# Kernel optimization log

Hardware: AMD Instinct MI355X
Metric: run time of the kernel (lower is better)

The kernel has to match this reference:

```python
import jax, jax.numpy as jnp
import numpy as np

B, N, K, F, L, H, ZMAX = 16, 1024, 16, 128, 4, 128, 100


def setup_inputs() -> dict:
    key = jax.random.key(0)
    ks = jax.random.split(key, 12)
    cell = jnp.eye(3, dtype=jnp.float32)[None] * 8.0 + 0.05 * jax.random.normal(ks[0], (B, 3, 3), dtype=jnp.float32)
    x = jax.random.uniform(ks[1], (B, N, 3), dtype=jnp.float32)
    z = jax.random.randint(ks[2], (B, N), 0, ZMAX)
    struct_size = jnp.full((B,), N, dtype=jnp.int32)
    emb = 0.02 * jax.random.normal(ks[3], (ZMAX, F), dtype=jnp.float32)
    din = 2 * F + 1
    W1 = jax.random.normal(ks[4], (L, din, F), dtype=jnp.float32) / np.sqrt(din)
    b1 = jnp.zeros((L, F), dtype=jnp.float32)
    W2 = jax.random.normal(ks[5], (L, F, F), dtype=jnp.float32) / np.sqrt(F)
    b2 = jnp.zeros((L, F), dtype=jnp.float32)
    A1 = jax.random.normal(ks[6], (din, H), dtype=jnp.float32) / np.sqrt(din)
    a1 = jnp.zeros((H,), dtype=jnp.float32)
    A2 = jax.random.normal(ks[7], (H, 1), dtype=jnp.float32) / np.sqrt(H)
    a2 = jnp.zeros((1,), dtype=jnp.float32)
    return {"cell": cell, "x": x, "z": z, "struct_size": struct_size, "emb": emb,
            "W1": W1, "b1": b1, "W2": W2, "b2": b2, "A1": A1, "a1": a1, "A2": A2, "a2": a2}


def _periodic_knn(cell, frac, k):
    # frac: [B,N,3] fractional coords, cell: [B,3,3] lattice rows.
    b, n, _ = frac.shape
    g = jnp.arange(-1, 2, dtype=frac.dtype)
    shifts = jnp.stack(jnp.meshgrid(g, g, g, indexing="ij"), -1).reshape(-1, 3)  # [27,3]
    rel = frac[:, None, :, :] - frac[:, :, None, :]  # rel[b,i,j] = frac_j - frac_i, [B,N,N,3]

    def body(carry, si):
        bd2, bsi = carry
        s, i = si
        cart = jnp.einsum("bijd,bde->bije", rel + s, cell)
        d2 = jnp.sum(cart * cart, axis=-1)
        upd = d2 < bd2
        return (jnp.where(upd, d2, bd2), jnp.where(upd, i, bsi)), None

    init = (jnp.full((b, n, n), 1e30, dtype=frac.dtype), jnp.zeros((b, n, n), dtype=jnp.int32))
    (d2min, simin), _ = jax.lax.scan(body, init, (shifts, jnp.arange(27, dtype=jnp.int32)))
    eye = jnp.eye(n, dtype=bool)
    d2min = jnp.where(eye[None], 1e30, d2min)  # exclude self (zero-shift) edges
    _, idx = jax.lax.top_k(-d2min, k)  # [B,N,k] neighbor indices
    sid = jnp.take_along_axis(simin, idx, axis=2)  # best image shift per edge
    svec = shifts[sid]  # [B,N,k,3]
    frac_j = jax.vmap(lambda f, i: f[i])(frac, idx)  # [B,N,k,3]
    vec = jnp.einsum("bnkd,bde->bnke", frac_j - frac[:, :, None, :] + svec, cell)
    d = jnp.sqrt(jnp.maximum(jnp.sum(vec * vec, axis=-1), 1e-12))  # [B,N,k]
    return idx, vec, d


def _edge_feat(h, idx, d):
    hj = jax.vmap(lambda hb, ib: hb[ib])(h, idx)  # [B,N,k,F]
    hi = jnp.broadcast_to(h[:, :, None, :], hj.shape)
    return jnp.concatenate([hi, hj, d[..., None]], axis=-1)  # [B,N,k,2F+1]


def reference(cell, x, z, struct_size, emb, W1, b1, W2, b2, A1, a1, A2, a2):
    frac = jnp.mod(x, 1.0)
    idx, vec, d = _periodic_knn(cell, frac, K)
    h = emb[z]  # [B,N,F]
    for l in range(W1.shape[0]):
        feat = _edge_feat(h, idx, d)
        m = jax.nn.silu(feat @ W1[l] + b1[l]) @ W2[l] + b2[l]  # [B,N,k,F]
        h = h + jnp.mean(m, axis=2)
    feat = _edge_feat(h, idx, d)
    w = jax.nn.silu(feat @ A1 + a1) @ A2 + a2  # [B,N,k,1]
    delta_cart = jnp.sum(w * vec, axis=2)  # [B,N,3]
    delta_frac = jnp.einsum("bnd,bde->bne", delta_cart, jnp.linalg.inv(cell))
    return x + delta_frac
```

## Files before the change

kernel.cpp:

```cpp
#include <hip/hip_runtime.h>

#define B_ 16
#define N_ 1024
#define K_ 16
#define F_ 128
#define L_ 4
#define DIN_ 257

typedef __bf16 bf16x8 __attribute__((ext_vector_type(8)));
typedef float f32x4 __attribute__((ext_vector_type(4)));

__device__ __forceinline__ float silu_f(float x) {
    return x / (1.0f + __expf(-x));
}

__device__ __forceinline__ unsigned short f2bf_bits(float f) {
    unsigned u = __builtin_bit_cast(unsigned, f);
    return (unsigned short)((u + 0x7FFFu + ((u >> 16) & 1u)) >> 16);
}

__global__ __launch_bounds__(256) void k_prep(const int* __restrict__ z,
                                              const float* __restrict__ emb,
                                              const float* __restrict__ W1,
                                              const float* __restrict__ W2,
                                              const float* __restrict__ A1,
                                              float* __restrict__ h,
                                              unsigned short* __restrict__ hbf,
                                              unsigned short* __restrict__ Wt1,
                                              unsigned short* __restrict__ Wt2,
                                              unsigned short* __restrict__ At1) {
    int gid = blockIdx.x * 256 + threadIdx.x;
    int id = gid;
    if (id < L_ * 256 * 128) {
        int k = id & 127, n = (id >> 7) & 255, l = id >> 15;
        float v = (n < 128) ? W1[(size_t)l * DIN_ * F_ + (size_t)k * F_ + n]
                            : W1[(size_t)l * DIN_ * F_ + (size_t)(128 + k) * F_ + (n - 128)];
        Wt1[id] = f2bf_bits(v);
    } else {
        int id2 = id - L_ * 256 * 128;
        if (id2 < L_ * 128 * 128) {
            int k = id2 & 127, n = (id2 >> 7) & 127, l = id2 >> 14;
            Wt2[id2] = f2bf_bits(W2[(size_t)l * F_ * F_ + (size_t)k * F_ + n]);
        } else {
            int id3 = id2 - L_ * 128 * 128;
            if (id3 < 256 * 128) {
                int k = id3 & 127, n = id3 >> 7;
                float v = (n < 128) ? A1[(size_t)k * 128 + n]
                                    : A1[(size_t)(128 + k) * 128 + (n - 128)];
                At1[id3] = f2bf_bits(v);
            }
        }
    }
    {
        int t = gid;
        int node = t >> 5;
        int f4 = (t & 31) << 2;
        int zi = z[node];
        float4 v = *reinterpret_cast<const float4*>(&emb[zi * F_ + f4]);
        *reinterpret_cast<float4*>(&h[node * F_ + f4]) = v;
        ushort4 pk;
        pk.x = f2bf_bits(v.x); pk.y = f2bf_bits(v.y);
        pk.z = f2bf_bits(v.z); pk.w = f2bf_bits(v.w);
        *reinterpret_cast<ushort4*>(&hbf[node * F_ + f4]) = pk;
    }
}

__global__ __launch_bounds__(256) void k_knng(const float* __restrict__ x,
                                              const float* __restrict__ cell,
                                              int* __restrict__ idx_o,
                                              float* __restrict__ vec_o,
                                              float* __restrict__ d_o,
                                              const unsigned short* __restrict__ hbf,
                                              const unsigned short* __restrict__ Wt1,
                                              float* __restrict__ uv0) {
    __shared__ float fr[N_ * 3];
    int tid = threadIdx.x;
    int gb = blockIdx.x;
    int batch = gb >> 6;
    int ib = gb & 63;
    const float* xb = x + batch * N_ * 3;
    for (int u = tid; u < N_ * 3; u += 256) {
        float xv = xb[u];
        fr[u] = xv - floorf(xv);
    }
    __syncthreads();
    int wave = tid >> 6;
    int lane = tid & 63;
    int fr16 = lane & 15, ko = lane >> 4;

    const float* cb = cell + batch * 9;
    float c00 = cb[0], c01 = cb[1], c02 = cb[2];
    float c10 = cb[3], c11 = cb[4], c12 = cb[5];
    float c20 = cb[6], c21 = cb[7], c22 = cb[8];

    for (int r4 = 0; r4 < 4; ++r4) {
        int i = ib * 16 + wave * 4 + r4;
        float fi0 = fr[i * 3 + 0], fi1 = fr[i * 3 + 1], fi2 = fr[i * 3 + 2];

        unsigned long long k[16];
#pragma unroll
        for (int t = 0; t < 16; ++t) {
            int j = t * 64 + lane;
            float r0 = fr[j * 3 + 0] - fi0;
            float r1 = fr[j * 3 + 1] - fi1;
            float r2 = fr[j * 3 + 2] - fi2;
            float s0f = (r0 > 0.f) ? -1.f : 0.f;
            float s1f = (r1 > 0.f) ? -1.f : 0.f;
            float s2f = (r2 > 0.f) ? -1.f : 0.f;
            int sid_base = ((r0 > 0.f) ? 0 : 9) + ((r1 > 0.f) ? 0 : 3) + ((r2 > 0.f) ? 0 : 1);
            float rx0 = r0 + s0f, rx1 = r0 + (s0f + 1.0f);
            float ry0 = r1 + s1f, ry1 = r1 + (s1f + 1.0f);
            float rz0 = r2 + s2f, rz1 = r2 + (s2f + 1.0f);
            float best = 3e38f;
            int bsid = 0;
#pragma unroll
            for (int cbo = 0; cbo < 8; ++cbo) {
                float rs0 = (cbo & 4) ? rx1 : rx0;
                float rs1 = (cbo & 2) ? ry1 : ry0;
                float rs2 = (cbo & 1) ? rz1 : rz0;
                float cx = fmaf(rs2, c20, fmaf(rs1, c10, rs0 * c00));
                float cy = fmaf(rs2, c21, fmaf(rs1, c11, rs0 * c01));
                float cz = fmaf(rs2, c22, fmaf(rs1, c12, rs0 * c02));
                float d2 = fmaf(cz, cz, fmaf(cy, cy, cx * cx));
                int sid = sid_base + ((cbo >> 2) & 1) * 9 + ((cbo >> 1) & 1) * 3 + (cbo & 1);
                if (d2 < best) { best = d2; bsid = sid; }
            }
            if (j == i) best = 3e38f;
            unsigned db = __builtin_bit_cast(unsigned, best);
            k[t] = ((unsigned long long)db << 32) | (unsigned)((j << 5) | bsid);
        }

#define CE_(a, b)                                              \
    {                                                          \
        unsigned long long x_ = k[a], y_ = k[b];               \
        bool s_ = y_ < x_;                                     \
        k[a] = s_ ? y_ : x_;                                   \
        k[b] = s_ ? x_ : y_;                                   \
    }
        CE_(0,1) CE_(2,3) CE_(4,5) CE_(6,7) CE_(8,9) CE_(10,11) CE_(12,13) CE_(14,15)
        CE_(0,2) CE_(1,3) CE_(4,6) CE_(5,7) CE_(8,10) CE_(9,11) CE_(12,14) CE_(13,15)
        CE_(1,2) CE_(5,6) CE_(9,10) CE_(13,14)
        CE_(0,4) CE_(1,5) CE_(2,6) CE_(3,7) CE_(8,12) CE_(9,13) CE_(10,14) CE_(11,15)
        CE_(2,4) CE_(3,5) CE_(10,12) CE_(11,13)
        CE_(1,2) CE_(3,4) CE_(5,6) CE_(9,10) CE_(11,12) CE_(13,14)
        CE_(0,8) CE_(1,9) CE_(2,10) CE_(3,11) CE_(4,12) CE_(5,13) CE_(6,14) CE_(7,15)
        CE_(4,8) CE_(5,9) CE_(6,10) CE_(7,11)
        CE_(2,4) CE_(3,5) CE_(6,8) CE_(7,9) CE_(10,12) CE_(11,13)
        CE_(1,2) CE_(3,4) CE_(5,6) CE_(7,8) CE_(9,10) CE_(11,12) CE_(13,14)
#undef CE_

        unsigned long long sel = 0;
        for (int r = 0; r < 16; ++r) {
            unsigned long long m = k[0];
#pragma unroll
            for (int off = 32; off >= 1; off >>= 1) {
                unsigned long long o = __shfl_xor(m, off);
                if (o < m) m = o;
            }
            if (k[0] == m) {
#pragma unroll
                for (int t = 0; t < 15; ++t) k[t] = k[t + 1];
                k[15] = ~0ull;
            }
            if (lane == r) sel = m;
        }

        if (lane < 16) {
            unsigned pk = (unsigned)sel;
            int j = pk >> 5, sid = pk & 31;
            int s0 = sid / 9 - 1, s1 = (sid / 3) % 3 - 1, s2 = sid % 3 - 1;
            float rs0 = (fr[j * 3 + 0] - fi0) + (float)s0;
            float rs1 = (fr[j * 3 + 1] - fi1) + (float)s1;
            float rs2 = (fr[j * 3 + 2] - fi2) + (float)s2;
            float vx = fmaf(rs2, c20, fmaf(rs1, c10, rs0 * c00));
            float vy = fmaf(rs2, c21, fmaf(rs1, c11, rs0 * c01));
            float vz = fmaf(rs2, c22, fmaf(rs1, c12, rs0 * c02));
            float d2 = fmaf(vz, vz, fmaf(vy, vy, vx * vx));
            float dd = sqrtf(fmaxf(d2, 1e-12f));
            int node = batch * N_ + i;
            int eo = node * K_ + lane;
            idx_o[eo] = j;
            d_o[eo] = dd;
            vec_o[eo * 3 + 0] = vx;
            vec_o[eo * 3 + 1] = vy;
            vec_o[eo * 3 + 2] = vz;
        }
    }

    {
        int t = gb * 4 + wave;
        int mt = t >> 3, nt = t & 7;
        const unsigned short* Ap = hbf + (size_t)(mt * 32 + fr16) * 128 + ko * 8;
        const unsigned short* Bp = Wt1 + (size_t)(nt * 32 + fr16) * 128 + ko * 8;
        bf16x8 a0[4], a1v_[4], b0[4], b1v_[4];
#pragma unroll
        for (int ks = 0; ks < 4; ++ks) {
            a0[ks] = *reinterpret_cast<const bf16x8*>(Ap + ks * 32);
            a1v_[ks] = *reinterpret_cast<const bf16x8*>(Ap + 16 * 128 + ks * 32);
            b0[ks] = *reinterpret_cast<const bf16x8*>(Bp + ks * 32);
            b1v_[ks] = *reinterpret_cast<const bf16x8*>(Bp + 16 * 128 + ks * 32);
        }
        f32x4 acc00 = {0.f, 0.f, 0.f, 0.f}, acc01 = acc00, acc10 = acc00, acc11 = acc00;
#pragma unroll
        for (int ks = 0; ks < 4; ++ks) {
            acc00 = __builtin_amdgcn_mfma_f32_16x16x32_bf16(a0[ks], b0[ks], acc00, 0, 0, 0);
            acc01 = __builtin_amdgcn_mfma_f32_16x16x32_bf16(a0[ks], b1v_[ks], acc01, 0, 0, 0);
            acc10 = __builtin_amdgcn_mfma_f32_16x16x32_bf16(a1v_[ks], b0[ks], acc10, 0, 0, 0);
            acc11 = __builtin_amdgcn_mfma_f32_16x16x32_bf16(a1v_[ks], b1v_[ks], acc11, 0, 0, 0);
        }
        int mrow = mt * 32 + ko * 4;
        int cbase = nt * 32 + fr16;
#define EPI_(FM, FN, ACC)                                                    \
    {                                                                        \
        int cc = cbase + FN * 16;                                            \
        _Pragma("unroll") for (int r = 0; r < 4; ++r) {                      \
            int row = mrow + FM * 16 + r;                                    \
            uv0[(size_t)row * 256 + cc] = ACC[r];                            \
        }                                                                    \
    }
        EPI_(0, 0, acc00) EPI_(0, 1, acc01) EPI_(1, 0, acc10) EPI_(1, 1, acc11)
#undef EPI_
    }
}

__global__ __launch_bounds__(256) void k_layer16(const float* __restrict__ UVin,
                                                 const int* __restrict__ idx,
                                                 const float* __restrict__ nd,
                                                 const float* __restrict__ w1d,
                                                 const float* __restrict__ b1l,
                                                 const unsigned short* __restrict__ W2t,
                                                 const float* __restrict__ b2l,
                                                 float* __restrict__ h,
                                                 const unsigned short* __restrict__ W1n,
                                                 float* __restrict__ UVout) {
    __shared__ unsigned short svl[16][136];
    __shared__ unsigned short hbl[16][136];
    __shared__ int ilds[256];
    __shared__ float dlds[256];
    int tid = threadIdx.x;
    int gb = blockIdx.x;
    int batch = (gb & 7) + 8 * (gb >> 9);
    int ib = (gb >> 3) & 63;
    int node0 = batch * N_ + ib * 16;
    int bbase = batch * N_;
    int wave = tid >> 6, lane = tid & 63;
    int fr16 = lane & 15, ko = lane >> 4;

    ilds[tid] = idx[node0 * K_ + tid];
    dlds[tid] = nd[node0 * K_ + tid];
    __syncthreads();

    {
        int gn = tid >> 4, fc = tid & 15, f0 = fc << 3;
        int node = node0 + gn;
        float u[8], wd[8], bb[8], acc[8];
#pragma unroll
        for (int q = 0; q < 8; q += 4) {
            float4 t = *reinterpret_cast<const float4*>(&UVin[(size_t)node * 256 + f0 + q]);
            u[q] = t.x; u[q + 1] = t.y; u[q + 2] = t.z; u[q + 3] = t.w;
            float4 t2 = *reinterpret_cast<const float4*>(&w1d[f0 + q]);
            wd[q] = t2.x; wd[q + 1] = t2.y; wd[q + 2] = t2.z; wd[q + 3] = t2.w;
            float4 t3 = *reinterpret_cast<const float4*>(&b1l[f0 + q]);
            bb[q] = t3.x; bb[q + 1] = t3.y; bb[q + 2] = t3.z; bb[q + 3] = t3.w;
        }
#pragma unroll
        for (int q = 0; q < 8; ++q) acc[q] = 0.f;
        for (int e = 0; e < K_; ++e) {
            int j = ilds[gn * K_ + e];
            float dd = dlds[gn * K_ + e];
            const float* vp = &UVin[(size_t)(bbase + j) * 256 + 128 + f0];
#pragma unroll
            for (int q = 0; q < 8; q += 4) {
                float4 t = *reinterpret_cast<const float4*>(&vp[q]);
                float v4[4] = {t.x, t.y, t.z, t.w};
#pragma unroll
                for (int w = 0; w < 4; ++w) {
                    float pre = u[q + w] + v4[w] + fmaf(dd, wd[q + w], bb[q + w]);
                    acc[q + w] += silu_f(pre);
                }
            }
        }
        const float inv_k = 1.0f / (float)K_;
        unsigned ow[4];
#pragma unroll
        for (int q = 0; q < 4; ++q)
            ow[q] = (unsigned)f2bf_bits(acc[2 * q] * inv_k) |
                    ((unsigned)f2bf_bits(acc[2 * q + 1] * inv_k) << 16);
        *reinterpret_cast<int4*>(&svl[gn][f0]) = make_int4(ow[0], ow[1], ow[2], ow[3]);
    }
    __syncthreads();

    {
        const unsigned short* Bp = W2t + (size_t)(wave * 32 + fr16) * 128 + ko * 8;
        bf16x8 a0[4], b0[4], b1f[4];
#pragma unroll
        for (int ks = 0; ks < 4; ++ks) {
            a0[ks] = *reinterpret_cast<const bf16x8*>(&svl[fr16][ks * 32 + ko * 8]);
            b0[ks] = *reinterpret_cast<const bf16x8*>(Bp + ks * 32);
            b1f[ks] = *reinterpret_cast<const bf16x8*>(Bp + 16 * 128 + ks * 32);
        }
        f32x4 acc00 = {0.f, 0.f, 0.f, 0.f}, acc01 = acc00;
#pragma unroll
        for (int ks = 0; ks < 4; ++ks) {
            acc00 = __builtin_amdgcn_mfma_f32_16x16x32_bf16(a0[ks], b0[ks], acc00, 0, 0, 0);
            acc01 = __builtin_amdgcn_mfma_f32_16x16x32_bf16(a0[ks], b1f[ks], acc01, 0, 0, 0);
        }
        int cb0 = wave * 32 + fr16;
#define EPI2_(FN, ACC)                                                         \
    {                                                                          \
        int col = cb0 + FN * 16;                                               \
        float bv = b2l[col];                                                   \
        _Pragma("unroll") for (int r = 0; r < 4; ++r) {                        \
            int row = ko * 4 + r;                                              \
            int grow = node0 + row;                                            \
            float val = ACC[r] + bv + h[(size_t)grow * 128 + col];             \
            h[(size_t)grow * 128 + col] = val;                                 \
            hbl[row][col] = f2bf_bits(val);                                    \
        }                                                                      \
    }
        EPI2_(0, acc00) EPI2_(1, acc01)
#undef EPI2_
    }
    __syncthreads();

#pragma unroll
    for (int half = 0; half < 2; ++half) {
        int nt2 = wave + half * 4;
        const unsigned short* Bp = W1n + (size_t)(nt2 * 32 + fr16) * 128 + ko * 8;
        bf16x8 a0[4], b0[4], b1f[4];
#pragma unroll
        for (int ks = 0; ks < 4; ++ks) {
            a0[ks] = *reinterpret_cast<const bf16x8*>(&hbl[fr16][ks * 32 + ko * 8]);
            b0[ks] = *reinterpret_cast<const bf16x8*>(Bp + ks * 32);
            b1f[ks] = *reinterpret_cast<const bf16x8*>(Bp + 16 * 128 + ks * 32);
        }
        f32x4 acc00 = {0.f, 0.f, 0.f, 0.f}, acc01 = acc00;
#pragma unroll
        for (int ks = 0; ks < 4; ++ks) {
            acc00 = __builtin_amdgcn_mfma_f32_16x16x32_bf16(a0[ks], b0[ks], acc00, 0, 0, 0);
            acc01 = __builtin_amdgcn_mfma_f32_16x16x32_bf16(a0[ks], b1f[ks], acc01, 0, 0, 0);
        }
        int cb0 = nt2 * 32 + fr16;
#define EPI1_(FN, ACC)                                                         \
    {                                                                          \
        int col = cb0 + FN * 16;                                               \
        _Pragma("unroll") for (int r = 0; r < 4; ++r) {                        \
            int row = ko * 4 + r;                                              \
            UVout[(size_t)(node0 + row) * 256 + col] = ACC[r];                 \
        }                                                                      \
    }
        EPI1_(0, acc00) EPI1_(1, acc01)
#undef EPI1_
    }
}

__global__ __launch_bounds__(256) void k_final(const float* __restrict__ P,
                                               const int* __restrict__ idx,
                                               const float* __restrict__ nd,
                                               const float* __restrict__ nvec,
                                               const float* __restrict__ A1d,
                                               const float* __restrict__ a1v,
                                               const float* __restrict__ A2v,
                                               const float* __restrict__ a2v,
                                               const float* __restrict__ x,
                                               const float* __restrict__ cell,
                                               float* __restrict__ out) {
    __shared__ float plds[16][256];
    __shared__ float wlds[16][17];
    __shared__ float dclds[16][3];
    int gb = blockIdx.x;
    int batch = (gb & 7) + 8 * (gb >> 9);
    int ib = (gb >> 3) & 63;
    int node0 = batch * N_ + ib * 16;
    int g = threadIdx.x >> 4, fc = threadIdx.x & 15;
    int node = node0 + g;
    int b = node >> 10;
    int f0 = fc * 8;
    float pa[8], ad[8], aa[8], a2r[8];
#pragma unroll
    for (int q = 0; q < 8; q += 4) {
        float4 t = *reinterpret_cast<const float4*>(&P[(size_t)node * 256 + f0 + q]);
        pa[q] = t.x; pa[q + 1] = t.y; pa[q + 2] = t.z; pa[q + 3] = t.w;
        float4 t2 = *reinterpret_cast<const float4*>(&A1d[f0 + q]);
        ad[q] = t2.x; ad[q + 1] = t2.y; ad[q + 2] = t2.z; ad[q + 3] = t2.w;
        float4 t3 = *reinterpret_cast<const float4*>(&a1v[f0 + q]);
        aa[q] = t3.x; aa[q + 1] = t3.y; aa[q + 2] = t3.z; aa[q + 3] = t3.w;
        float4 t4 = *reinterpret_cast<const float4*>(&A2v[f0 + q]);
        a2r[q] = t4.x; a2r[q + 1] = t4.y; a2r[q + 2] = t4.z; a2r[q + 3] = t4.w;
    }
    int ebase = node * K_;
    for (int e = 0; e < K_; ++e) {
        int j = idx[ebase + e];
        float dd = nd[ebase + e];
        const float* vp = &P[(size_t)(b * N_ + j) * 256 + 128 + f0];
        float part = 0.f;
#pragma unroll
        for (int q = 0; q < 8; q += 4) {
            float4 t = *reinterpret_cast<const float4*>(&vp[q]);
            float v4[4] = {t.x, t.y, t.z, t.w};
#pragma unroll
            for (int w = 0; w < 4; ++w) {
                float pre = pa[q + w] + v4[w] + fmaf(dd, ad[q + w], aa[q + w]);
                part = fmaf(silu_f(pre), a2r[q + w], part);
            }
        }
        plds[e][(g << 4) | fc] = part;
    }
    __syncthreads();
    {
        int g2 = threadIdx.x >> 4, e2 = threadIdx.x & 15;
        float w = a2v[0];
#pragma unroll
        for (int f2 = 0; f2 < 16; ++f2) w += plds[e2][(g2 << 4) | f2];
        wlds[g2][e2] = w;
    }
    __syncthreads();
    if (threadIdx.x < 48) {
        int gg = threadIdx.x & 15, c = threadIdx.x >> 4;
        int noded = node0 + gg;
        float dc = 0.f;
#pragma unroll
        for (int e = 0; e < K_; ++e)
            dc = fmaf(wlds[gg][e], nvec[(size_t)(noded * K_ + e) * 3 + c], dc);
        dclds[gg][c] = dc;
    }
    __syncthreads();
    if (threadIdx.x < 48) {
        int gg = threadIdx.x & 15, c = threadIdx.x >> 4;
        int noded = node0 + gg;
        int bb2 = noded >> 10;
        const float* cb = cell + bb2 * 9;
        float c00 = cb[0], c01 = cb[1], c02 = cb[2];
        float c10 = cb[3], c11 = cb[4], c12 = cb[5];
        float c20 = cb[6], c21 = cb[7], c22 = cb[8];
        float det = c00 * (c11 * c22 - c12 * c21) - c01 * (c10 * c22 - c12 * c20) +
                    c02 * (c10 * c21 - c11 * c20);
        float rdet = 1.0f / det;
        float i0c, i1c, i2c;
        if (c == 0) {
            i0c = (c11 * c22 - c12 * c21) * rdet;
            i1c = -(c10 * c22 - c12 * c20) * rdet;
            i2c = (c10 * c21 - c11 * c20) * rdet;
        } else if (c == 1) {
            i0c = -(c01 * c22 - c02 * c21) * rdet;
            i1c = (c00 * c22 - c02 * c20) * rdet;
            i2c = -(c00 * c21 - c01 * c20) * rdet;
        } else {
            i0c = (c01 * c12 - c02 * c11) * rdet;
            i1c = -(c00 * c12 - c02 * c10) * rdet;
            i2c = (c00 * c11 - c01 * c10) * rdet;
        }
        float df = dclds[gg][0] * i0c + dclds[gg][1] * i1c + dclds[gg][2] * i2c;
        out[(size_t)noded * 3 + c] = x[(size_t)noded * 3 + c] + df;
    }
}

extern "C" void kernel_launch(void* const* d_in, const int* in_sizes, int n_in,
                              void* d_out, int out_size, void* d_ws, size_t ws_size,
                              hipStream_t stream) {
    (void)in_sizes; (void)n_in; (void)out_size; (void)ws_size;
    const float* cell = (const float*)d_in[0];
    const float* x    = (const float*)d_in[1];
    const int*   z    = (const int*)d_in[2];
    const float* emb  = (const float*)d_in[4];
    const float* W1   = (const float*)d_in[5];
    const float* b1   = (const float*)d_in[6];
    const float* W2   = (const float*)d_in[7];
    const float* b2   = (const float*)d_in[8];
    const float* A1   = (const float*)d_in[9];
    const float* a1   = (const float*)d_in[10];
    const float* A2   = (const float*)d_in[11];
    const float* a2   = (const float*)d_in[12];
    float* out = (float*)d_out;

    char* ws = (char*)d_ws;
    size_t off = 0;
    auto alloc = [&](size_t bytes) {
        void* p = ws + off;
        off = (off + bytes + 255) & ~(size_t)255;
        return p;
    };
    int* idx    = (int*)alloc((size_t)B_ * N_ * K_ * 4);
    float* nd   = (float*)alloc((size_t)B_ * N_ * K_ * 4);
    float* nvec = (float*)alloc((size_t)B_ * N_ * K_ * 3 * 4);
    float* h0   = (float*)alloc((size_t)B_ * N_ * F_ * 4);
    float* uv0  = (float*)alloc((size_t)B_ * N_ * 256 * 4);
    float* uv1  = (float*)alloc((size_t)B_ * N_ * 256 * 4);
    unsigned short* hbf = (unsigned short*)alloc((size_t)B_ * N_ * F_ * 2);
    unsigned short* Wt1 = (unsigned short*)alloc((size_t)L_ * 256 * 128 * 2);
    unsigned short* Wt2 = (unsigned short*)alloc((size_t)L_ * 128 * 128 * 2);
    unsigned short* At1 = (unsigned short*)alloc((size_t)256 * 128 * 2);

    k_prep<<<2048, 256, 0, stream>>>(z, emb, W1, W2, A1, h0, hbf, Wt1, Wt2, At1);
    k_knng<<<1024, 256, 0, stream>>>(x, cell, idx, nvec, nd, hbf, Wt1, uv0);

    for (int l = 0; l < L_; ++l) {
        const float* uin = (l & 1) ? uv1 : uv0;
        float* uout = (l & 1) ? uv0 : uv1;
        const unsigned short* W1next = (l < 3) ? (Wt1 + (size_t)(l + 1) * 256 * 128) : At1;
        k_layer16<<<1024, 256, 0, stream>>>(uin, idx, nd,
                                            W1 + (size_t)l * DIN_ * F_ + 256 * F_,
                                            b1 + l * F_, Wt2 + (size_t)l * 128 * 128,
                                            b2 + l * F_, h0, W1next, uout);
    }
    k_final<<<1024, 256, 0, stream>>>(uv0, idx, nd, nvec, A1 + 256 * F_, a1, A2, a2, x, cell,
                                      out);
}
```

Measured before the change: 273.5 us.

## Split kNN and first GEMM into separate kernels; batch neighbor gathers

Splits the fused kNN plus layer-0 GEMM kernel into a standalone bf16 MFMA GEMM kernel and a kNN kernel with one query row per wave. The kNN kernel now launches four times as many blocks, each reloading the batch's fractional coordinates into shared memory, which trades redundant loads for more parallelism. The layer and final kernels read neighbor indices and distances as int4/float4 vectors in registers instead of staging them in LDS, which removes a barrier. They also issue four neighbor row gathers before computing, to get more memory-level parallelism at some cost in register pressure.

```diff
diff --git a/kernel.cpp b/kernel.cpp
--- a/kernel.cpp
+++ b/kernel.cpp
@@ -65,70 +65,62 @@
     }
 }
 
-__global__ __launch_bounds__(256) void k_knng(const float* __restrict__ x,
-                                              const float* __restrict__ cell,
-                                              int* __restrict__ idx_o,
-                                              float* __restrict__ vec_o,
-                                              float* __restrict__ d_o,
-                                              const unsigned short* __restrict__ hbf,
-                                              const unsigned short* __restrict__ Wt1,
-                                              float* __restrict__ uv0) {
+__global__ __launch_bounds__(256) void k_knn(const float* __restrict__ x,
+                                             const float* __restrict__ cell,
+                                             int* __restrict__ idx_o,
+                                             float* __restrict__ vec_o,
+                                             float* __restrict__ d_o) {
     __shared__ float fr[N_ * 3];
-    int tid = threadIdx.x;
-    int gb = blockIdx.x;
-    int batch = gb >> 6;
-    int ib = gb & 63;
-    const float* xb = x + batch * N_ * 3;
-    for (int u = tid; u < N_ * 3; u += 256) {
+    int b = blockIdx.x >> 8;
+    int ib = (blockIdx.x & 255) << 2;
+    const float* xb = x + b * N_ * 3;
+    for (int u = threadIdx.x; u < N_ * 3; u += 256) {
         float xv = xb[u];
         fr[u] = xv - floorf(xv);
     }
     __syncthreads();
-    int wave = tid >> 6;
-    int lane = tid & 63;
-    int fr16 = lane & 15, ko = lane >> 4;
-
-    const float* cb = cell + batch * 9;
+    int wave = threadIdx.x >> 6;
+    int lane = threadIdx.x & 63;
+    int i = ib + wave;
+
+    const float* cb = cell + b * 9;
     float c00 = cb[0], c01 = cb[1], c02 = cb[2];
     float c10 = cb[3], c11 = cb[4], c12 = cb[5];
     float c20 = cb[6], c21 = cb[7], c22 = cb[8];
-
-    for (int r4 = 0; r4 < 4; ++r4) {
-        int i = ib * 16 + wave * 4 + r4;
-        float fi0 = fr[i * 3 + 0], fi1 = fr[i * 3 + 1], fi2 = fr[i * 3 + 2];
-
-        unsigned long long k[16];
-#pragma unroll
-        for (int t = 0; t < 16; ++t) {
-            int j = t * 64 + lane;
-            float r0 = fr[j * 3 + 0] - fi0;
-            float r1 = fr[j * 3 + 1] - fi1;
-            float r2 = fr[j * 3 + 2] - fi2;
-            float s0f = (r0 > 0.f) ? -1.f : 0.f;
-            float s1f = (r1 > 0.f) ? -1.f : 0.f;
-            float s2f = (r2 > 0.f) ? -1.f : 0.f;
-            int sid_base = ((r0 > 0.f) ? 0 : 9) + ((r1 > 0.f) ? 0 : 3) + ((r2 > 0.f) ? 0 : 1);
-            float rx0 = r0 + s0f, rx1 = r0 + (s0f + 1.0f);
-            float ry0 = r1 + s1f, ry1 = r1 + (s1f + 1.0f);
-            float rz0 = r2 + s2f, rz1 = r2 + (s2f + 1.0f);
-            float best = 3e38f;
-            int bsid = 0;
-#pragma unroll
-            for (int cbo = 0; cbo < 8; ++cbo) {
-                float rs0 = (cbo & 4) ? rx1 : rx0;
-                float rs1 = (cbo & 2) ? ry1 : ry0;
-                float rs2 = (cbo & 1) ? rz1 : rz0;
-                float cx = fmaf(rs2, c20, fmaf(rs1, c10, rs0 * c00));
-                float cy = fmaf(rs2, c21, fmaf(rs1, c11, rs0 * c01));
-                float cz = fmaf(rs2, c22, fmaf(rs1, c12, rs0 * c02));
-                float d2 = fmaf(cz, cz, fmaf(cy, cy, cx * cx));
-                int sid = sid_base + ((cbo >> 2) & 1) * 9 + ((cbo >> 1) & 1) * 3 + (cbo & 1);
-                if (d2 < best) { best = d2; bsid = sid; }
-            }
-            if (j == i) best = 3e38f;
-            unsigned db = __builtin_bit_cast(unsigned, best);
-            k[t] = ((unsigned long long)db << 32) | (unsigned)((j << 5) | bsid);
-        }
+    float fi0 = fr[i * 3 + 0], fi1 = fr[i * 3 + 1], fi2 = fr[i * 3 + 2];
+
+    unsigned long long k[16];
+#pragma unroll
+    for (int t = 0; t < 16; ++t) {
+        int j = t * 64 + lane;
+        float r0 = fr[j * 3 + 0] - fi0;
+        float r1 = fr[j * 3 + 1] - fi1;
+        float r2 = fr[j * 3 + 2] - fi2;
+        float s0f = (r0 > 0.f) ? -1.f : 0.f;
+        float s1f = (r1 > 0.f) ? -1.f : 0.f;
+        float s2f = (r2 > 0.f) ? -1.f : 0.f;
+        int sid_base = ((r0 > 0.f) ? 0 : 9) + ((r1 > 0.f) ? 0 : 3) + ((r2 > 0.f) ? 0 : 1);
+        float rx0 = r0 + s0f, rx1 = r0 + (s0f + 1.0f);
+        float ry0 = r1 + s1f, ry1 = r1 + (s1f + 1.0f);
+        float rz0 = r2 + s2f, rz1 = r2 + (s2f + 1.0f);
+        float best = 3e38f;
+        int bsid = 0;
+#pragma unroll
+        for (int cbo = 0; cbo < 8; ++cbo) {
+            float rs0 = (cbo & 4) ? rx1 : rx0;
+            float rs1 = (cbo & 2) ? ry1 : ry0;
+            float rs2 = (cbo & 1) ? rz1 : rz0;
+            float cx = fmaf(rs2, c20, fmaf(rs1, c10, rs0 * c00));
+            float cy = fmaf(rs2, c21, fmaf(rs1, c11, rs0 * c01));
+            float cz = fmaf(rs2, c22, fmaf(rs1, c12, rs0 * c02));
+            float d2 = fmaf(cz, cz, fmaf(cy, cy, cx * cx));
+            int sid = sid_base + ((cbo >> 2) & 1) * 9 + ((cbo >> 1) & 1) * 3 + (cbo & 1);
+            if (d2 < best) { best = d2; bsid = sid; }
+        }
+        if (j == i) best = 3e38f;
+        unsigned db = __builtin_bit_cast(unsigned, best);
+        k[t] = ((unsigned long long)db << 32) | (unsigned)((j << 5) | bsid);
+    }
 
 #define CE_(a, b)                                              \
     {                                                          \
@@ -137,90 +129,94 @@
         k[a] = s_ ? y_ : x_;                                   \
         k[b] = s_ ? x_ : y_;                                   \
     }
-        CE_(0,1) CE_(2,3) CE_(4,5) CE_(6,7) CE_(8,9) CE_(10,11) CE_(12,13) CE_(14,15)
-        CE_(0,2) CE_(1,3) CE_(4,6) CE_(5,7) CE_(8,10) CE_(9,11) CE_(12,14) CE_(13,15)
-        CE_(1,2) CE_(5,6) CE_(9,10) CE_(13,14)
-        CE_(0,4) CE_(1,5) CE_(2,6) CE_(3,7) CE_(8,12) CE_(9,13) CE_(10,14) CE_(11,15)
-        CE_(2,4) CE_(3,5) CE_(10,12) CE_(11,13)
-        CE_(1,2) CE_(3,4) CE_(5,6) CE_(9,10) CE_(11,12) CE_(13,14)
-        CE_(0,8) CE_(1,9) CE_(2,10) CE_(3,11) CE_(4,12) CE_(5,13) CE_(6,14) CE_(7,15)
-        CE_(4,8) CE_(5,9) CE_(6,10) CE_(7,11)
-        CE_(2,4) CE_(3,5) CE_(6,8) CE_(7,9) CE_(10,12) CE_(11,13)
-        CE_(1,2) CE_(3,4) CE_(5,6) CE_(7,8) CE_(9,10) CE_(11,12) CE_(13,14)
+    CE_(0,1) CE_(2,3) CE_(4,5) CE_(6,7) CE_(8,9) CE_(10,11) CE_(12,13) CE_(14,15)
+    CE_(0,2) CE_(1,3) CE_(4,6) CE_(5,7) CE_(8,10) CE_(9,11) CE_(12,14) CE_(13,15)
+    CE_(1,2) CE_(5,6) CE_(9,10) CE_(13,14)
+    CE_(0,4) CE_(1,5) CE_(2,6) CE_(3,7) CE_(8,12) CE_(9,13) CE_(10,14) CE_(11,15)
+    CE_(2,4) CE_(3,5) CE_(10,12) CE_(11,13)
+    CE_(1,2) CE_(3,4) CE_(5,6) CE_(9,10) CE_(11,12) CE_(13,14)
+    CE_(0,8) CE_(1,9) CE_(2,10) CE_(3,11) CE_(4,12) CE_(5,13) CE_(6,14) CE_(7,15)
+    CE_(4,8) CE_(5,9) CE_(6,10) CE_(7,11)
+    CE_(2,4) CE_(3,5) CE_(6,8) CE_(7,9) CE_(10,12) CE_(11,13)
+    CE_(1,2) CE_(3,4) CE_(5,6) CE_(7,8) CE_(9,10) CE_(11,12) CE_(13,14)
 #undef CE_
 
-        unsigned long long sel = 0;
-        for (int r = 0; r < 16; ++r) {
-            unsigned long long m = k[0];
-#pragma unroll
-            for (int off = 32; off >= 1; off >>= 1) {
-                unsigned long long o = __shfl_xor(m, off);
-                if (o < m) m = o;
-            }
-            if (k[0] == m) {
-#pragma unroll
-                for (int t = 0; t < 15; ++t) k[t] = k[t + 1];
-                k[15] = ~0ull;
-            }
-            if (lane == r) sel = m;
-        }
-
-        if (lane < 16) {
-            unsigned pk = (unsigned)sel;
-            int j = pk >> 5, sid = pk & 31;
-            int s0 = sid / 9 - 1, s1 = (sid / 3) % 3 - 1, s2 = sid % 3 - 1;
-            float rs0 = (fr[j * 3 + 0] - fi0) + (float)s0;
-            float rs1 = (fr[j * 3 + 1] - fi1) + (float)s1;
-            float rs2 = (fr[j * 3 + 2] - fi2) + (float)s2;
-            float vx = fmaf(rs2, c20, fmaf(rs1, c10, rs0 * c00));
-            float vy = fmaf(rs2, c21, fmaf(rs1, c11, rs0 * c01));
-            float vz = fmaf(rs2, c22, fmaf(rs1, c12, rs0 * c02));
-            float d2 = fmaf(vz, vz, fmaf(vy, vy, vx * vx));
-            float dd = sqrtf(fmaxf(d2, 1e-12f));
-            int node = batch * N_ + i;
-            int eo = node * K_ + lane;
-            idx_o[eo] = j;
-            d_o[eo] = dd;
-            vec_o[eo * 3 + 0] = vx;
-            vec_o[eo * 3 + 1] = vy;
-            vec_o[eo * 3 + 2] = vz;
-        }
-    }
-
-    {
-        int t = gb * 4 + wave;
-        int mt = t >> 3, nt = t & 7;
-        const unsigned short* Ap = hbf + (size_t)(mt * 32 + fr16) * 128 + ko * 8;
-        const unsigned short* Bp = Wt1 + (size_t)(nt * 32 + fr16) * 128 + ko * 8;
-        bf16x8 a0[4], a1v_[4], b0[4], b1v_[4];
-#pragma unroll
-        for (int ks = 0; ks < 4; ++ks) {
-            a0[ks] = *reinterpret_cast<const bf16x8*>(Ap + ks * 32);
-            a1v_[ks] = *reinterpret_cast<const bf16x8*>(Ap + 16 * 128 + ks * 32);
-            b0[ks] = *reinterpret_cast<const bf16x8*>(Bp + ks * 32);
-            b1v_[ks] = *reinterpret_cast<const bf16x8*>(Bp + 16 * 128 + ks * 32);
-        }
-        f32x4 acc00 = {0.f, 0.f, 0.f, 0.f}, acc01 = acc00, acc10 = acc00, acc11 = acc00;
-#pragma unroll
-        for (int ks = 0; ks < 4; ++ks) {
-            acc00 = __builtin_amdgcn_mfma_f32_16x16x32_bf16(a0[ks], b0[ks], acc00, 0, 0, 0);
-            acc01 = __builtin_amdgcn_mfma_f32_16x16x32_bf16(a0[ks], b1v_[ks], acc01, 0, 0, 0);
-            acc10 = __builtin_amdgcn_mfma_f32_16x16x32_bf16(a1v_[ks], b0[ks], acc10, 0, 0, 0);
-            acc11 = __builtin_amdgcn_mfma_f32_16x16x32_bf16(a1v_[ks], b1v_[ks], acc11, 0, 0, 0);
-        }
-        int mrow = mt * 32 + ko * 4;
-        int cbase = nt * 32 + fr16;
+    unsigned long long sel = 0;
+    for (int r = 0; r < 16; ++r) {
+        unsigned long long m = k[0];
+#pragma unroll
+        for (int off = 32; off >= 1; off >>= 1) {
+            unsigned long long o = __shfl_xor(m, off);
+            if (o < m) m = o;
+        }
+        if (k[0] == m) {
+#pragma unroll
+            for (int t = 0; t < 15; ++t) k[t] = k[t + 1];
+            k[15] = ~0ull;
+        }
+        if (lane == r) sel = m;
+    }
+
+    if (lane < 16) {
+        unsigned pk = (unsigned)sel;
+        int j = pk >> 5, sid = pk & 31;
+        int s0 = sid / 9 - 1, s1 = (sid / 3) % 3 - 1, s2 = sid % 3 - 1;
+        float rs0 = (fr[j * 3 + 0] - fi0) + (float)s0;
+        float rs1 = (fr[j * 3 + 1] - fi1) + (float)s1;
+        float rs2 = (fr[j * 3 + 2] - fi2) + (float)s2;
+        float vx = fmaf(rs2, c20, fmaf(rs1, c10, rs0 * c00));
+        float vy = fmaf(rs2, c21, fmaf(rs1, c11, rs0 * c01));
+        float vz = fmaf(rs2, c22, fmaf(rs1, c12, rs0 * c02));
+        float d2 = fmaf(vz, vz, fmaf(vy, vy, vx * vx));
+        float dd = sqrtf(fmaxf(d2, 1e-12f));
+        int node = b * N_ + i;
+        int eo = node * K_ + lane;
+        idx_o[eo] = j;
+        d_o[eo] = dd;
+        vec_o[eo * 3 + 0] = vx;
+        vec_o[eo * 3 + 1] = vy;
+        vec_o[eo * 3 + 2] = vz;
+    }
+}
+
+__global__ __launch_bounds__(256) void k_wgemm(const unsigned short* __restrict__ A,
+                                               const unsigned short* __restrict__ Bt,
+                                               float* __restrict__ C) {
+    int wave = threadIdx.x >> 6, lane = threadIdx.x & 63;
+    int tile = blockIdx.x * 4 + wave;
+    int mt = tile >> 3, nt = tile & 7;
+    int fr16 = lane & 15, ko = lane >> 4;
+    const unsigned short* Ap = A + (size_t)(mt * 32 + fr16) * 128 + ko * 8;
+    const unsigned short* Bp = Bt + (size_t)(nt * 32 + fr16) * 128 + ko * 8;
+
+    bf16x8 a0[4], a1[4], b0[4], b1[4];
+#pragma unroll
+    for (int ks = 0; ks < 4; ++ks) {
+        a0[ks] = *reinterpret_cast<const bf16x8*>(Ap + ks * 32);
+        a1[ks] = *reinterpret_cast<const bf16x8*>(Ap + 16 * 128 + ks * 32);
+        b0[ks] = *reinterpret_cast<const bf16x8*>(Bp + ks * 32);
+        b1[ks] = *reinterpret_cast<const bf16x8*>(Bp + 16 * 128 + ks * 32);
+    }
+    f32x4 acc00 = {0.f, 0.f, 0.f, 0.f}, acc01 = acc00, acc10 = acc00, acc11 = acc00;
+#pragma unroll
+    for (int ks = 0; ks < 4; ++ks) {
+        acc00 = __builtin_amdgcn_mfma_f32_16x16x32_bf16(a0[ks], b0[ks], acc00, 0, 0, 0);
+        acc01 = __builtin_amdgcn_mfma_f32_16x16x32_bf16(a0[ks], b1[ks], acc01, 0, 0, 0);
+        acc10 = __builtin_amdgcn_mfma_f32_16x16x32_bf16(a1[ks], b0[ks], acc10, 0, 0, 0);
+        acc11 = __builtin_amdgcn_mfma_f32_16x16x32_bf16(a1[ks], b1[ks], acc11, 0, 0, 0);
+    }
+    int mrow = mt * 32 + ko * 4;
+    int cbase = nt * 32 + fr16;
 #define EPI_(FM, FN, ACC)                                                    \
     {                                                                        \
         int cc = cbase + FN * 16;                                            \
         _Pragma("unroll") for (int r = 0; r < 4; ++r) {                      \
             int row = mrow + FM * 16 + r;                                    \
-            uv0[(size_t)row * 256 + cc] = ACC[r];                            \
+            C[(size_t)row * 256 + cc] = ACC[r];                              \
         }                                                                    \
     }
-        EPI_(0, 0, acc00) EPI_(0, 1, acc01) EPI_(1, 0, acc10) EPI_(1, 1, acc11)
+    EPI_(0, 0, acc00) EPI_(0, 1, acc01) EPI_(1, 0, acc10) EPI_(1, 1, acc11)
 #undef EPI_
-    }
 }
 
 __global__ __launch_bounds__(256) void k_layer16(const float* __restrict__ UVin,
@@ -235,8 +231,6 @@
                                                  float* __restrict__ UVout) {
     __shared__ unsigned short svl[16][136];
     __shared__ unsigned short hbl[16][136];
-    __shared__ int ilds[256];
-    __shared__ float dlds[256];
     int tid = threadIdx.x;
     int gb = blockIdx.x;
     int batch = (gb & 7) + 8 * (gb >> 9);
@@ -246,13 +240,16 @@
     int wave = tid >> 6, lane = tid & 63;
     int fr16 = lane & 15, ko = lane >> 4;
 
-    ilds[tid] = idx[node0 * K_ + tid];
-    dlds[tid] = nd[node0 * K_ + tid];
-    __syncthreads();
-
     {
         int gn = tid >> 4, fc = tid & 15, f0 = fc << 3;
         int node = node0 + gn;
+        int4 ji[4];
+        float4 di[4];
+#pragma unroll
+        for (int q = 0; q < 4; ++q) {
+            ji[q] = *reinterpret_cast<const int4*>(&idx[node * K_ + q * 4]);
+            di[q] = *reinterpret_cast<const float4*>(&nd[node * K_ + q * 4]);
+        }
         float u[8], wd[8], bb[8], acc[8];
 #pragma unroll
         for (int q = 0; q < 8; q += 4) {
@@ -265,18 +262,26 @@
         }
 #pragma unroll
         for (int q = 0; q < 8; ++q) acc[q] = 0.f;
-        for (int e = 0; e < K_; ++e) {
-            int j = ilds[gn * K_ + e];
-            float dd = dlds[gn * K_ + e];
-            const float* vp = &UVin[(size_t)(bbase + j) * 256 + 128 + f0];
-#pragma unroll
-            for (int q = 0; q < 8; q += 4) {
-                float4 t = *reinterpret_cast<const float4*>(&vp[q]);
-                float v4[4] = {t.x, t.y, t.z, t.w};
-#pragma unroll
-                for (int w = 0; w < 4; ++w) {
-                    float pre = u[q + w] + v4[w] + fmaf(dd, wd[q + w], bb[q + w]);
-                    acc[q + w] += silu_f(pre);
+#pragma unroll
+        for (int eq = 0; eq < 4; ++eq) {
+            int j4[4] = {ji[eq].x, ji[eq].y, ji[eq].z, ji[eq].w};
+            float d4[4] = {di[eq].x, di[eq].y, di[eq].z, di[eq].w};
+            float4 va[4], vb[4];
+#pragma unroll
+            for (int e = 0; e < 4; ++e) {
+                const float* vp = &UVin[(size_t)(bbase + j4[e]) * 256 + 128 + f0];
+                va[e] = *reinterpret_cast<const float4*>(&vp[0]);
+                vb[e] = *reinterpret_cast<const float4*>(&vp[4]);
+            }
+#pragma unroll
+            for (int e = 0; e < 4; ++e) {
+                float dd = d4[e];
+                float v8[8] = {va[e].x, va[e].y, va[e].z, va[e].w,
+                               vb[e].x, vb[e].y, vb[e].z, vb[e].w};
+#pragma unroll
+                for (int w = 0; w < 8; ++w) {
+                    float pre = u[w] + v8[w] + fmaf(dd, wd[w], bb[w]);
+                    acc[w] += silu_f(pre);
                 }
             }
         }
@@ -372,10 +377,17 @@
     int batch = (gb & 7) + 8 * (gb >> 9);
     int ib = (gb >> 3) & 63;
     int node0 = batch * N_ + ib * 16;
+    int bbase = batch * N_;
     int g = threadIdx.x >> 4, fc = threadIdx.x & 15;
     int node = node0 + g;
-    int b = node >> 10;
     int f0 = fc * 8;
+    int4 ji[4];
+    float4 di[4];
+#pragma unroll
+    for (int q = 0; q < 4; ++q) {
+        ji[q] = *reinterpret_cast<const int4*>(&idx[node * K_ + q * 4]);
+        di[q] = *reinterpret_cast<const float4*>(&nd[node * K_ + q * 4]);
+    }
     float pa[8], ad[8], aa[8], a2r[8];
 #pragma unroll
     for (int q = 0; q < 8; q += 4) {
@@ -388,23 +400,30 @@
         float4 t4 = *reinterpret_cast<const float4*>(&A2v[f0 + q]);
         a2r[q] = t4.x; a2r[q + 1] = t4.y; a2r[q + 2] = t4.z; a2r[q + 3] = t4.w;
     }
-    int ebase = node * K_;
-    for (int e = 0; e < K_; ++e) {
-        int j = idx[ebase + e];
-        float dd = nd[ebase + e];
-        const float* vp = &P[(size_t)(b * N_ + j) * 256 + 128 + f0];
-        float part = 0.f;
-#pragma unroll
-        for (int q = 0; q < 8; q += 4) {
-            float4 t = *reinterpret_cast<const float4*>(&vp[q]);
-            float v4[4] = {t.x, t.y, t.z, t.w};
-#pragma unroll
-            for (int w = 0; w < 4; ++w) {
-                float pre = pa[q + w] + v4[w] + fmaf(dd, ad[q + w], aa[q + w]);
-                part = fmaf(silu_f(pre), a2r[q + w], part);
+#pragma unroll
+    for (int eq = 0; eq < 4; ++eq) {
+        int j4[4] = {ji[eq].x, ji[eq].y, ji[eq].z, ji[eq].w};
+        float d4[4] = {di[eq].x, di[eq].y, di[eq].z, di[eq].w};
+        float4 va[4], vb[4];
+#pragma unroll
+        for (int e = 0; e < 4; ++e) {
+            const float* vp = &P[(size_t)(bbase + j4[e]) * 256 + 128 + f0];
+            va[e] = *reinterpret_cast<const float4*>(&vp[0]);
+            vb[e] = *reinterpret_cast<const float4*>(&vp[4]);
+        }
+#pragma unroll
+        for (int e = 0; e < 4; ++e) {
+            float dd = d4[e];
+            float v8[8] = {va[e].x, va[e].y, va[e].z, va[e].w,
+                           vb[e].x, vb[e].y, vb[e].z, vb[e].w};
+            float part = 0.f;
+#pragma unroll
+            for (int w = 0; w < 8; ++w) {
+                float pre = pa[w] + v8[w] + fmaf(dd, ad[w], aa[w]);
+                part = fmaf(silu_f(pre), a2r[w], part);
             }
-        }
-        plds[e][(g << 4) | fc] = part;
+            plds[eq * 4 + e][(g << 4) | fc] = part;
+        }
     }
     __syncthreads();
     {
@@ -428,8 +447,7 @@
     if (threadIdx.x < 48) {
         int gg = threadIdx.x & 15, c = threadIdx.x >> 4;
         int noded = node0 + gg;
-        int bb2 = noded >> 10;
-        const float* cb = cell + bb2 * 9;
+        const float* cb = cell + batch * 9;
         float c00 = cb[0], c01 = cb[1], c02 = cb[2];
         float c10 = cb[3], c11 = cb[4], c12 = cb[5];
         float c20 = cb[6], c21 = cb[7], c22 = cb[8];
@@ -492,7 +510,8 @@
     unsigned short* At1 = (unsigned short*)alloc((size_t)256 * 128 * 2);
 
     k_prep<<<2048, 256, 0, stream>>>(z, emb, W1, W2, A1, h0, hbf, Wt1, Wt2, At1);
-    k_knng<<<1024, 256, 0, stream>>>(x, cell, idx, nvec, nd, hbf, Wt1, uv0);
+    k_wgemm<<<1024, 256, 0, stream>>>(hbf, Wt1, uv0);
+    k_knn<<<4096, 256, 0, stream>>>(x, cell, idx, nvec, nd);
 
     for (int l = 0; l < L_; ++l) {
         const float* uin = (l & 1) ? uv1 : uv0;
```

Measured after the change: 273.3 us. No clear change (-0.1%).
